# Kernel tuning notes

Hardware: AMD Instinct MI355X
Metric: run time of the kernel (lower is better)

Reference implementation:

```python
import jax, jax.numpy as jnp
import numpy as np

NUM_FIELDS = 40
EMBED_DIM = 128
BATCH = 1024
NUM_IX = NUM_FIELDS * (NUM_FIELDS - 1) // 2  # 780


def _pair_indices(num_fields):
    row, col = [], []
    for i in range(num_fields - 1):
        for j in range(i + 1, num_fields):
            row.append(i)
            col.append(j)
    return np.asarray(row, dtype=np.int32), np.asarray(col, dtype=np.int32)


def setup_inputs() -> dict:
    key = jax.random.key(0)
    k1, k2 = jax.random.split(key)
    x = jax.random.normal(k1, (BATCH, NUM_FIELDS, EMBED_DIM), dtype=jnp.float32)
    # 'mat' kernel: (embed_dim, num_ix, embed_dim), random_normal init
    kernel = jax.random.normal(k2, (EMBED_DIM, NUM_IX, EMBED_DIM), dtype=jnp.float32) * 0.05
    return {"x": x, "kernel": kernel}


def reference(x, kernel) -> jnp.ndarray:
    # x: (B, F, D); kernel: (D, num_ix, D)
    row, col = _pair_indices(x.shape[1])
    p = x[:, row, :]  # (B, num_ix, D)
    q = x[:, col, :]  # (B, num_ix, D)
    # Original: tmp[b,e,n] = sum_d p[b,n,d]*kernel[e,n,d]; kp[b,n] = sum_e tmp[b,e,n]*q[b,n,e]
    # Fused contraction, never materializing the (B, D, num_ix, D) tensor:
    kp = jnp.einsum('bnd,end,bne->bn', p, kernel, q)
    return kp  # (B, num_ix)
```

## Files before the change

### kernel.cpp

```cpp
#include <hip/hip_runtime.h>

#define NF 40
#define ED 128
#define NB 1024
#define NIX 780
#define XROW (NF * ED)
#define KROW (NIX * ED)
#define XB_BYTES (NB * NF * ED * 2)
#define KB_BYTES (NIX * ED * ED * 2)
#define WS_NEED (XB_BYTES + KB_BYTES)

typedef __attribute__((ext_vector_type(8))) short bf16x8;
typedef __attribute__((ext_vector_type(4))) float f32x4;
typedef __attribute__((ext_vector_type(4))) unsigned short ushx4;
typedef __attribute__((ext_vector_type(8))) unsigned short ushx8;

__device__ __forceinline__ unsigned short f2bf(float x) {
  unsigned int u = __float_as_uint(x);
  u = (u + 0x7FFFu + ((u >> 16) & 1u)) >> 16;
  return (unsigned short)u;
}
__device__ __forceinline__ float bf2f(unsigned short h) {
  return __uint_as_float(((unsigned int)h) << 16);
}

#define GLOAD16(gsrc, ldst)                                                    \
  __builtin_amdgcn_global_load_lds(                                            \
      (const __attribute__((address_space(1))) void*)(gsrc),                   \
      (__attribute__((address_space(3))) void*)(ldst), 16, 0, 0)

__global__ void cvt_x(const float* __restrict__ x, unsigned short* __restrict__ xb) {
  const size_t g = ((size_t)blockIdx.x * 256 + threadIdx.x) * 8;
  float4 a = *reinterpret_cast<const float4*>(x + g);
  float4 b = *reinterpret_cast<const float4*>(x + g + 4);
  ushx8 h;
  h[0] = f2bf(a.x); h[1] = f2bf(a.y); h[2] = f2bf(a.z); h[3] = f2bf(a.w);
  h[4] = f2bf(b.x); h[5] = f2bf(b.y); h[6] = f2bf(b.z); h[7] = f2bf(b.w);
  *reinterpret_cast<ushx8*>(xb + g) = h;
}

__global__ void cvt_k(const float* __restrict__ kr, unsigned short* __restrict__ kb) {
  const size_t g = ((size_t)blockIdx.x * 256 + threadIdx.x) * 4;
  const int d = (int)(g & 127);
  const size_t t = g >> 7;
  const int e = (int)(t & 127);
  const int n = (int)(t >> 7);
  float4 v = *reinterpret_cast<const float4*>(kr + ((size_t)e * NIX + n) * ED + d);
  ushx4 h;
  h[0] = f2bf(v.x); h[1] = f2bf(v.y); h[2] = f2bf(v.z); h[3] = f2bf(v.w);
  *reinterpret_cast<ushx4*>(kb + g) = h;
}

__launch_bounds__(256, 2)
__global__ void opn_ws(const unsigned short* __restrict__ xb,
                       const unsigned short* __restrict__ kb,
                       float* __restrict__ out) {
  __shared__ unsigned short S[128 * 128];
  unsigned short* Klds = S;
  unsigned short* Plds = S;
  unsigned short* Qlds = S + 8192;

  const int n = blockIdx.x;
  const int tid = threadIdx.x;
  const int lane = tid & 63;
  const int w = tid >> 6;
  const int lm = lane & 15;
  const int lq = lane >> 4;
  const int col8 = lm * 8;

  int fi = 0, base = 0;
  while (base + (NF - 1 - fi) <= n) { base += NF - 1 - fi; ++fi; }
  const int fj = fi + 1 + (n - base);

  {
    const unsigned short* ks = kb + (size_t)n * (ED * ED);
    #pragma unroll
    for (int j = 0; j < 8; ++j) {
      const int chunk = j * 4 + w;
      const int r = chunk * 4 + lq;
      const int c = col8 ^ ((r & 7) << 3);
      GLOAD16(ks + r * ED + c, Klds + chunk * 512);
    }
  }
  __syncthreads();

  bf16x8 afr[4][8];
  #pragma unroll
  for (int kk = 0; kk < 4; ++kk)
    #pragma unroll
    for (int f = 0; f < 8; ++f) {
      const int r = f * 16 + lm;
      afr[kk][f] = *reinterpret_cast<const bf16x8*>(
          &Klds[r * ED + ((kk * 32 + lq * 8) ^ ((r & 7) << 3))]);
    }
  #pragma unroll
  for (int kk = 0; kk < 4; ++kk)
    #pragma unroll
    for (int f = 0; f < 8; ++f)
      asm volatile("" : "+v"(afr[kk][f]));
  __syncthreads();

  for (int t = 0; t < 8; ++t) {
    const int b0 = blockIdx.y * 512 + t * 64;

    #pragma unroll
    for (int j = 0; j < 4; ++j) {
      const int chunk = j * 4 + w;
      const int r = chunk * 4 + lq;
      const int c = col8 ^ ((r & 7) << 3);
      const size_t xoff = ((size_t)(b0 + r) * NF) * ED + c;
      GLOAD16(xb + xoff + (size_t)fi * ED, Plds + chunk * 512);
      GLOAD16(xb + xoff + (size_t)fj * ED, Qlds + chunk * 512);
    }
    __syncthreads();

    f32x4 acc[8];
    #pragma unroll
    for (int f = 0; f < 8; ++f) acc[f] = (f32x4){0.f, 0.f, 0.f, 0.f};
    const int prow = w * 16 + lm;
    #pragma unroll
    for (int kk = 0; kk < 4; ++kk) {
      bf16x8 pfr = *reinterpret_cast<const bf16x8*>(
          &Plds[prow * ED + ((kk * 32 + lq * 8) ^ ((prow & 7) << 3))]);
      #pragma unroll
      for (int f = 0; f < 8; ++f)
        acc[f] = __builtin_amdgcn_mfma_f32_16x16x32_bf16(afr[kk][f], pfr, acc[f], 0, 0, 0);
    }

    float s = 0.f;
    #pragma unroll
    for (int f = 0; f < 8; ++f) {
      const int c = (f * 16 + lq * 4) ^ ((prow & 7) << 3);
      ushx4 q4 = *reinterpret_cast<const ushx4*>(&Qlds[prow * ED + c]);
      #pragma unroll
      for (int r = 0; r < 4; ++r)
        s = fmaf(acc[f][r], bf2f(q4[r]), s);
    }
    s += __shfl_xor(s, 16);
    s += __shfl_xor(s, 32);
    if (lane < 16) out[(size_t)(b0 + prow) * NIX + n] = s;
    __syncthreads();
  }
}

__device__ __forceinline__ int swz_fb(int row, int col) {
  return row * 128 + (col ^ ((row & 7) << 3));
}

__launch_bounds__(256, 2)
__global__ void opn_fb(const float* __restrict__ x,
                       const float* __restrict__ kern,
                       float* __restrict__ out) {
  __shared__ unsigned short Klds[128 * 128];
  __shared__ unsigned short Plds[64 * 128];
  __shared__ unsigned short Qlds[64 * 132];

  const int n = blockIdx.x;
  const int tid = threadIdx.x;
  const int lane = tid & 63;
  const int w = tid >> 6;
  const int lm = lane & 15;
  const int lq = lane >> 4;

  int fi = 0, base = 0;
  while (base + (NF - 1 - fi) <= n) { base += NF - 1 - fi; ++fi; }
  const int fj = fi + 1 + (n - base);

  {
    const int r8 = tid >> 5;
    const int d0 = (tid & 31) * 4;
    const float* kbp = kern + (size_t)n * ED + d0;
    #pragma unroll
    for (int p = 0; p < 16; ++p) {
      int e = p * 8 + r8;
      float4 v = *reinterpret_cast<const float4*>(kbp + (size_t)e * KROW);
      ushx4 h;
      h[0] = f2bf(v.x); h[1] = f2bf(v.y); h[2] = f2bf(v.z); h[3] = f2bf(v.w);
      *reinterpret_cast<ushx4*>(&Klds[swz_fb(e, d0)]) = h;
    }
  }
  __syncthreads();

  bf16x8 bfr[4][8];
  #pragma unroll
  for (int kk = 0; kk < 4; ++kk)
    #pragma unroll
    for (int f = 0; f < 8; ++f)
      bfr[kk][f] = *reinterpret_cast<const bf16x8*>(
          &Klds[swz_fb(f * 16 + lm, kk * 32 + lq * 8)]);

  const int r8 = tid >> 5;
  const int c4 = (tid & 31) * 4;

  for (int t = 0; t < 8; ++t) {
    const int b0 = blockIdx.y * 512 + t * 64;
    __syncthreads();
    #pragma unroll
    for (int p = 0; p < 8; ++p) {
      int r = p * 8 + r8;
      const float* xbp = x + (size_t)(b0 + r) * XROW + c4;
      float4 vp = *reinterpret_cast<const float4*>(xbp + fi * ED);
      ushx4 hp;
      hp[0] = f2bf(vp.x); hp[1] = f2bf(vp.y); hp[2] = f2bf(vp.z); hp[3] = f2bf(vp.w);
      *reinterpret_cast<ushx4*>(&Plds[swz_fb(r, c4)]) = hp;
      float4 vq = *reinterpret_cast<const float4*>(xbp + fj * ED);
      ushx4 hq;
      hq[0] = f2bf(vq.x); hq[1] = f2bf(vq.y); hq[2] = f2bf(vq.z); hq[3] = f2bf(vq.w);
      *reinterpret_cast<ushx4*>(&Qlds[r * 132 + c4]) = hq;
    }
    __syncthreads();

    f32x4 acc[8];
    #pragma unroll
    for (int f = 0; f < 8; ++f) acc[f] = (f32x4){0.f, 0.f, 0.f, 0.f};
    #pragma unroll
    for (int kk = 0; kk < 4; ++kk) {
      bf16x8 a = *reinterpret_cast<const bf16x8*>(
          &Plds[swz_fb(w * 16 + lm, kk * 32 + lq * 8)]);
      #pragma unroll
      for (int f = 0; f < 8; ++f)
        acc[f] = __builtin_amdgcn_mfma_f32_16x16x32_bf16(a, bfr[kk][f], acc[f], 0, 0, 0);
    }

    #pragma unroll
    for (int r = 0; r < 4; ++r) {
      const int bl = w * 16 + lq * 4 + r;
      float s = 0.f;
      #pragma unroll
      for (int f = 0; f < 8; ++f)
        s = fmaf(acc[f][r], bf2f(Qlds[bl * 132 + f * 16 + lm]), s);
      s += __shfl_xor(s, 1);
      s += __shfl_xor(s, 2);
      s += __shfl_xor(s, 4);
      s += __shfl_xor(s, 8);
      if (lm == 0) out[(size_t)(b0 + bl) * NIX + n] = s;
    }
  }
}

extern "C" void kernel_launch(void* const* d_in, const int* in_sizes, int n_in,
                              void* d_out, int out_size, void* d_ws, size_t ws_size,
                              hipStream_t stream) {
  const float* x = (const float*)d_in[0];
  const float* kern = (const float*)d_in[1];
  float* out = (float*)d_out;
  (void)in_sizes; (void)n_in; (void)out_size;

  if (ws_size >= (size_t)WS_NEED) {
    unsigned short* xb = (unsigned short*)d_ws;
    unsigned short* kbuf = (unsigned short*)((char*)d_ws + XB_BYTES);
    cvt_x<<<2560, 256, 0, stream>>>(x, xb);
    cvt_k<<<12480, 256, 0, stream>>>(kern, kbuf);
    dim3 grid(NIX, 2, 1);
    opn_ws<<<grid, 256, 0, stream>>>(xb, kbuf, out);
  } else {
    dim3 grid(NIX, 2, 1);
    opn_fb<<<grid, 256, 0, stream>>>(x, kern, out);
  }
}
```

Before: 76.26 us.

## Double-buffer P/Q tile loads in LDS to overlap global loads with MFMA

Doubles LDS to two 32KB buffers and software-pipelines the batch-tile loop so the next tile's P/Q rows are loaded asynchronously via global_load_lds while the current tile is computed. It replaces __syncthreads with explicit vmcnt waits and raw barriers, and overlaps the first tile load with the kernel-matrix load. This targets load latency stalls between tiles, at the cost of 64KB LDS per block, which may limit occupancy to the launch-bounds target of 2 blocks and relies on correct vmcnt counting.

```diff
diff --git a/kernel.cpp b/kernel.cpp
--- a/kernel.cpp
+++ b/kernel.cpp
@@ -28,6 +28,15 @@
   __builtin_amdgcn_global_load_lds(                                            \
       (const __attribute__((address_space(1))) void*)(gsrc),                   \
       (__attribute__((address_space(3))) void*)(ldst), 16, 0, 0)
+
+#define WAITV(N) asm volatile("s_waitcnt vmcnt(" #N ")" ::: "memory")
+#define WAITL0() asm volatile("s_waitcnt lgkmcnt(0)" ::: "memory")
+#define BARRIER()                                                              \
+  do {                                                                         \
+    asm volatile("" ::: "memory");                                             \
+    __builtin_amdgcn_s_barrier();                                              \
+    asm volatile("" ::: "memory");                                             \
+  } while (0)
 
 __global__ void cvt_x(const float* __restrict__ x, unsigned short* __restrict__ xb) {
   const size_t g = ((size_t)blockIdx.x * 256 + threadIdx.x) * 8;
@@ -55,10 +64,9 @@
 __global__ void opn_ws(const unsigned short* __restrict__ xb,
                        const unsigned short* __restrict__ kb,
                        float* __restrict__ out) {
-  __shared__ unsigned short S[128 * 128];
-  unsigned short* Klds = S;
-  unsigned short* Plds = S;
-  unsigned short* Qlds = S + 8192;
+  __shared__ unsigned short S[32768];
+  unsigned short* buf0 = S;
+  unsigned short* buf1 = S + 16384;
 
   const int n = blockIdx.x;
   const int tid = threadIdx.x;
@@ -72,6 +80,10 @@
   while (base + (NF - 1 - fi) <= n) { base += NF - 1 - fi; ++fi; }
   const int fj = fi + 1 + (n - base);
 
+  const unsigned short* xpi = xb + (size_t)fi * ED;
+  const unsigned short* xpj = xb + (size_t)fj * ED;
+  const int b0base = blockIdx.y * 512;
+
   {
     const unsigned short* ks = kb + (size_t)n * (ED * ED);
     #pragma unroll
@@ -79,41 +91,48 @@
       const int chunk = j * 4 + w;
       const int r = chunk * 4 + lq;
       const int c = col8 ^ ((r & 7) << 3);
-      GLOAD16(ks + r * ED + c, Klds + chunk * 512);
-    }
-  }
-  __syncthreads();
-
-  bf16x8 afr[4][8];
-  #pragma unroll
-  for (int kk = 0; kk < 4; ++kk)
-    #pragma unroll
-    for (int f = 0; f < 8; ++f) {
-      const int r = f * 16 + lm;
-      afr[kk][f] = *reinterpret_cast<const bf16x8*>(
-          &Klds[r * ED + ((kk * 32 + lq * 8) ^ ((r & 7) << 3))]);
-    }
-  #pragma unroll
-  for (int kk = 0; kk < 4; ++kk)
-    #pragma unroll
-    for (int f = 0; f < 8; ++f)
-      asm volatile("" : "+v"(afr[kk][f]));
-  __syncthreads();
-
-  for (int t = 0; t < 8; ++t) {
-    const int b0 = blockIdx.y * 512 + t * 64;
-
+      GLOAD16(ks + r * ED + c, buf1 + chunk * 512);
+    }
+  }
+
+  auto stage_pq = [&](unsigned short* buf, int t) {
+    const int b0 = b0base + t * 64;
     #pragma unroll
     for (int j = 0; j < 4; ++j) {
       const int chunk = j * 4 + w;
       const int r = chunk * 4 + lq;
       const int c = col8 ^ ((r & 7) << 3);
-      const size_t xoff = ((size_t)(b0 + r) * NF) * ED + c;
-      GLOAD16(xb + xoff + (size_t)fi * ED, Plds + chunk * 512);
-      GLOAD16(xb + xoff + (size_t)fj * ED, Qlds + chunk * 512);
-    }
-    __syncthreads();
-
+      const size_t xoff = (size_t)(b0 + r) * XROW + c;
+      GLOAD16(xpi + xoff, buf + chunk * 512);
+      GLOAD16(xpj + xoff, buf + 8192 + chunk * 512);
+    }
+  };
+
+  stage_pq(buf0, 0);
+  WAITV(8);
+  BARRIER();
+
+  bf16x8 afr[4][8];
+  #pragma unroll
+  for (int kk = 0; kk < 4; ++kk)
+    #pragma unroll
+    for (int f = 0; f < 8; ++f) {
+      const int r = f * 16 + lm;
+      afr[kk][f] = *reinterpret_cast<const bf16x8*>(
+          &buf1[r * ED + ((kk * 32 + lq * 8) ^ ((r & 7) << 3))]);
+    }
+  #pragma unroll
+  for (int kk = 0; kk < 4; ++kk)
+    #pragma unroll
+    for (int f = 0; f < 8; ++f)
+      asm volatile("" : "+v"(afr[kk][f]));
+  WAITL0();
+  BARRIER();
+
+  auto compute = [&](const unsigned short* buf, int t) {
+    const unsigned short* Pl = buf;
+    const unsigned short* Ql = buf + 8192;
+    const int b0 = b0base + t * 64;
     f32x4 acc[8];
     #pragma unroll
     for (int f = 0; f < 8; ++f) acc[f] = (f32x4){0.f, 0.f, 0.f, 0.f};
@@ -121,17 +140,16 @@
     #pragma unroll
     for (int kk = 0; kk < 4; ++kk) {
       bf16x8 pfr = *reinterpret_cast<const bf16x8*>(
-          &Plds[prow * ED + ((kk * 32 + lq * 8) ^ ((prow & 7) << 3))]);
+          &Pl[prow * ED + ((kk * 32 + lq * 8) ^ ((prow & 7) << 3))]);
       #pragma unroll
       for (int f = 0; f < 8; ++f)
         acc[f] = __builtin_amdgcn_mfma_f32_16x16x32_bf16(afr[kk][f], pfr, acc[f], 0, 0, 0);
     }
-
     float s = 0.f;
     #pragma unroll
     for (int f = 0; f < 8; ++f) {
       const int c = (f * 16 + lq * 4) ^ ((prow & 7) << 3);
-      ushx4 q4 = *reinterpret_cast<const ushx4*>(&Qlds[prow * ED + c]);
+      ushx4 q4 = *reinterpret_cast<const ushx4*>(&Ql[prow * ED + c]);
       #pragma unroll
       for (int r = 0; r < 4; ++r)
         s = fmaf(acc[f][r], bf2f(q4[r]), s);
@@ -139,8 +157,29 @@
     s += __shfl_xor(s, 16);
     s += __shfl_xor(s, 32);
     if (lane < 16) out[(size_t)(b0 + prow) * NIX + n] = s;
-    __syncthreads();
-  }
+  };
+
+  #pragma unroll 1
+  for (int t = 0; t < 6; t += 2) {
+    stage_pq(buf1, t + 1);
+    WAITV(8);
+    BARRIER();
+    compute(buf0, t);
+    BARRIER();
+    stage_pq(buf0, t + 2);
+    WAITV(8);
+    BARRIER();
+    compute(buf1, t + 1);
+    BARRIER();
+  }
+  stage_pq(buf1, 7);
+  WAITV(8);
+  BARRIER();
+  compute(buf0, 6);
+  BARRIER();
+  WAITV(0);
+  BARRIER();
+  compute(buf1, 7);
 }
 
 __device__ __forceinline__ int swz_fb(int row, int col) {
```

After: 68.37 us. 10.4% less time.

## Fuse conversion kernels and load P/Q directly from global with register double-buffering

Applied to the files above, without the earlier changes.

Merges the x and kernel bf16 conversion kernels into one launch, removing one kernel launch and the gap between them. In the main kernel, P and Q rows are no longer staged through LDS with barriers. Each lane reads its MFMA operand fragments straight from global memory into registers, and the next batch tile's P fragment is prefetched while the current tile computes. This drops the per-tile __syncthreads and LDS traffic, at the cost of less coalesced global reads and higher register pressure.

```diff
diff --git a/kernel.cpp b/kernel.cpp
--- a/kernel.cpp
+++ b/kernel.cpp
@@ -29,36 +29,35 @@
       (const __attribute__((address_space(1))) void*)(gsrc),                   \
       (__attribute__((address_space(3))) void*)(ldst), 16, 0, 0)
 
-__global__ void cvt_x(const float* __restrict__ x, unsigned short* __restrict__ xb) {
-  const size_t g = ((size_t)blockIdx.x * 256 + threadIdx.x) * 8;
-  float4 a = *reinterpret_cast<const float4*>(x + g);
-  float4 b = *reinterpret_cast<const float4*>(x + g + 4);
-  ushx8 h;
-  h[0] = f2bf(a.x); h[1] = f2bf(a.y); h[2] = f2bf(a.z); h[3] = f2bf(a.w);
-  h[4] = f2bf(b.x); h[5] = f2bf(b.y); h[6] = f2bf(b.z); h[7] = f2bf(b.w);
-  *reinterpret_cast<ushx8*>(xb + g) = h;
-}
-
-__global__ void cvt_k(const float* __restrict__ kr, unsigned short* __restrict__ kb) {
-  const size_t g = ((size_t)blockIdx.x * 256 + threadIdx.x) * 4;
-  const int d = (int)(g & 127);
-  const size_t t = g >> 7;
-  const int e = (int)(t & 127);
-  const int n = (int)(t >> 7);
-  float4 v = *reinterpret_cast<const float4*>(kr + ((size_t)e * NIX + n) * ED + d);
-  ushx4 h;
-  h[0] = f2bf(v.x); h[1] = f2bf(v.y); h[2] = f2bf(v.z); h[3] = f2bf(v.w);
-  *reinterpret_cast<ushx4*>(kb + g) = h;
+__global__ void cvt_fused(const float* __restrict__ x, const float* __restrict__ kr,
+                          unsigned short* __restrict__ xb, unsigned short* __restrict__ kb) {
+  const int blk = blockIdx.x;
+  if (blk < 2560) {
+    const size_t g = ((size_t)blk * 256 + threadIdx.x) * 8;
+    float4 a = *reinterpret_cast<const float4*>(x + g);
+    float4 b = *reinterpret_cast<const float4*>(x + g + 4);
+    ushx8 h;
+    h[0] = f2bf(a.x); h[1] = f2bf(a.y); h[2] = f2bf(a.z); h[3] = f2bf(a.w);
+    h[4] = f2bf(b.x); h[5] = f2bf(b.y); h[6] = f2bf(b.z); h[7] = f2bf(b.w);
+    *reinterpret_cast<ushx8*>(xb + g) = h;
+  } else {
+    const size_t g = ((size_t)(blk - 2560) * 256 + threadIdx.x) * 4;
+    const int d = (int)(g & 127);
+    const size_t t = g >> 7;
+    const int e = (int)(t & 127);
+    const int n = (int)(t >> 7);
+    float4 v = *reinterpret_cast<const float4*>(kr + ((size_t)e * NIX + n) * ED + d);
+    ushx4 h;
+    h[0] = f2bf(v.x); h[1] = f2bf(v.y); h[2] = f2bf(v.z); h[3] = f2bf(v.w);
+    *reinterpret_cast<ushx4*>(kb + g) = h;
+  }
 }
 
 __launch_bounds__(256, 2)
 __global__ void opn_ws(const unsigned short* __restrict__ xb,
                        const unsigned short* __restrict__ kb,
                        float* __restrict__ out) {
-  __shared__ unsigned short S[128 * 128];
-  unsigned short* Klds = S;
-  unsigned short* Plds = S;
-  unsigned short* Qlds = S + 8192;
+  __shared__ unsigned short Klds[ED * ED];
 
   const int n = blockIdx.x;
   const int tid = threadIdx.x;
@@ -66,7 +65,6 @@
   const int w = tid >> 6;
   const int lm = lane & 15;
   const int lq = lane >> 4;
-  const int col8 = lm * 8;
 
   int fi = 0, base = 0;
   while (base + (NF - 1 - fi) <= n) { base += NF - 1 - fi; ++fi; }
@@ -74,6 +72,7 @@
 
   {
     const unsigned short* ks = kb + (size_t)n * (ED * ED);
+    const int col8 = lm * 8;
     #pragma unroll
     for (int j = 0; j < 8; ++j) {
       const int chunk = j * 4 + w;
@@ -98,48 +97,55 @@
     #pragma unroll
     for (int f = 0; f < 8; ++f)
       asm volatile("" : "+v"(afr[kk][f]));
-  __syncthreads();
-
-  for (int t = 0; t < 8; ++t) {
-    const int b0 = blockIdx.y * 512 + t * 64;
-
-    #pragma unroll
-    for (int j = 0; j < 4; ++j) {
-      const int chunk = j * 4 + w;
-      const int r = chunk * 4 + lq;
-      const int c = col8 ^ ((r & 7) << 3);
-      const size_t xoff = ((size_t)(b0 + r) * NF) * ED + c;
-      GLOAD16(xb + xoff + (size_t)fi * ED, Plds + chunk * 512);
-      GLOAD16(xb + xoff + (size_t)fj * ED, Qlds + chunk * 512);
-    }
-    __syncthreads();
+
+  const int prow = w * 16 + lm;
+  const int row0 = blockIdx.y * 512 + prow;
+  const unsigned short* pP = xb + (size_t)fi * ED + (size_t)row0 * XROW + lq * 8;
+  const unsigned short* pQ = xb + (size_t)fj * ED + (size_t)row0 * XROW + lq * 4;
+  float* po = out + (size_t)row0 * NIX + n;
+
+  auto loadP = [&](bf16x8 (&pf)[4], int t) {
+    const unsigned short* p = pP + (size_t)t * (64 * XROW);
+    #pragma unroll
+    for (int kk = 0; kk < 4; ++kk)
+      pf[kk] = *reinterpret_cast<const bf16x8*>(p + kk * 32);
+  };
+
+  auto body = [&](bf16x8 (&pf)[4], int t) {
+    const unsigned short* q = pQ + (size_t)t * (64 * XROW);
+    ushx4 qv[8];
+    #pragma unroll
+    for (int f = 0; f < 8; ++f)
+      qv[f] = *reinterpret_cast<const ushx4*>(q + f * 16);
 
     f32x4 acc[8];
     #pragma unroll
     for (int f = 0; f < 8; ++f) acc[f] = (f32x4){0.f, 0.f, 0.f, 0.f};
-    const int prow = w * 16 + lm;
-    #pragma unroll
-    for (int kk = 0; kk < 4; ++kk) {
-      bf16x8 pfr = *reinterpret_cast<const bf16x8*>(
-          &Plds[prow * ED + ((kk * 32 + lq * 8) ^ ((prow & 7) << 3))]);
+    #pragma unroll
+    for (int kk = 0; kk < 4; ++kk)
       #pragma unroll
       for (int f = 0; f < 8; ++f)
-        acc[f] = __builtin_amdgcn_mfma_f32_16x16x32_bf16(afr[kk][f], pfr, acc[f], 0, 0, 0);
-    }
+        acc[f] = __builtin_amdgcn_mfma_f32_16x16x32_bf16(afr[kk][f], pf[kk], acc[f], 0, 0, 0);
 
     float s = 0.f;
     #pragma unroll
-    for (int f = 0; f < 8; ++f) {
-      const int c = (f * 16 + lq * 4) ^ ((prow & 7) << 3);
-      ushx4 q4 = *reinterpret_cast<const ushx4*>(&Qlds[prow * ED + c]);
+    for (int f = 0; f < 8; ++f)
       #pragma unroll
       for (int r = 0; r < 4; ++r)
-        s = fmaf(acc[f][r], bf2f(q4[r]), s);
-    }
+        s = fmaf(acc[f][r], bf2f(qv[f][r]), s);
     s += __shfl_xor(s, 16);
     s += __shfl_xor(s, 32);
-    if (lane < 16) out[(size_t)(b0 + prow) * NIX + n] = s;
-    __syncthreads();
+    if (lane < 16) po[(size_t)t * (64 * NIX)] = s;
+  };
+
+  bf16x8 pA[4], pB[4];
+  loadP(pA, 0);
+  #pragma unroll 1
+  for (int t = 0; t < 8; t += 2) {
+    loadP(pB, t + 1);
+    body(pA, t);
+    if (t + 2 < 8) loadP(pA, t + 2);
+    body(pB, t + 1);
   }
 }
 
@@ -249,8 +255,7 @@
   if (ws_size >= (size_t)WS_NEED) {
     unsigned short* xb = (unsigned short*)d_ws;
     unsigned short* kbuf = (unsigned short*)((char*)d_ws + XB_BYTES);
-    cvt_x<<<2560, 256, 0, stream>>>(x, xb);
-    cvt_k<<<12480, 256, 0, stream>>>(kern, kbuf);
+    cvt_fused<<<15040, 256, 0, stream>>>(x, kern, xb, kbuf);
     dim3 grid(NIX, 2, 1);
     opn_ws<<<grid, 256, 0, stream>>>(xb, kbuf, out);
   } else {
```

New measurement: 108.4 us. 42.1% more time.

## Split kernel columns across waves, shrink batch tile, fuse conversion launches

Applied to the files above, without the earlier changes.

The two bf16 conversion kernels are merged into one launch that branches on block index, removing one kernel launch and its tail. In the main kernel each wave now keeps only its own 32-row slice of the per-pair kernel matrix in registers instead of all 128 rows. Partial dot products are combined across waves through a small shared scratch array. This cuts register pressure so occupancy can rise to 4 blocks per CU, and the batch tile per block and grid are reshaped so twice as many blocks run. The cost is that each pair's kernel matrix is fetched by twice as many blocks, plus an extra cross-wave reduction with a barrier per tile.

```diff
diff --git a/kernel.cpp b/kernel.cpp
--- a/kernel.cpp
+++ b/kernel.cpp
@@ -29,36 +29,36 @@
       (const __attribute__((address_space(1))) void*)(gsrc),                   \
       (__attribute__((address_space(3))) void*)(ldst), 16, 0, 0)
 
-__global__ void cvt_x(const float* __restrict__ x, unsigned short* __restrict__ xb) {
-  const size_t g = ((size_t)blockIdx.x * 256 + threadIdx.x) * 8;
-  float4 a = *reinterpret_cast<const float4*>(x + g);
-  float4 b = *reinterpret_cast<const float4*>(x + g + 4);
-  ushx8 h;
-  h[0] = f2bf(a.x); h[1] = f2bf(a.y); h[2] = f2bf(a.z); h[3] = f2bf(a.w);
-  h[4] = f2bf(b.x); h[5] = f2bf(b.y); h[6] = f2bf(b.z); h[7] = f2bf(b.w);
-  *reinterpret_cast<ushx8*>(xb + g) = h;
-}
-
-__global__ void cvt_k(const float* __restrict__ kr, unsigned short* __restrict__ kb) {
-  const size_t g = ((size_t)blockIdx.x * 256 + threadIdx.x) * 4;
-  const int d = (int)(g & 127);
-  const size_t t = g >> 7;
-  const int e = (int)(t & 127);
-  const int n = (int)(t >> 7);
-  float4 v = *reinterpret_cast<const float4*>(kr + ((size_t)e * NIX + n) * ED + d);
-  ushx4 h;
-  h[0] = f2bf(v.x); h[1] = f2bf(v.y); h[2] = f2bf(v.z); h[3] = f2bf(v.w);
-  *reinterpret_cast<ushx4*>(kb + g) = h;
-}
-
-__launch_bounds__(256, 2)
+__global__ void cvt_fused(const float* __restrict__ x, const float* __restrict__ kr,
+                          unsigned short* __restrict__ xb, unsigned short* __restrict__ kb) {
+  const int blk = blockIdx.x;
+  if (blk < 2560) {
+    const size_t g = ((size_t)blk * 256 + threadIdx.x) * 8;
+    float4 a = *reinterpret_cast<const float4*>(x + g);
+    float4 b = *reinterpret_cast<const float4*>(x + g + 4);
+    ushx8 h;
+    h[0] = f2bf(a.x); h[1] = f2bf(a.y); h[2] = f2bf(a.z); h[3] = f2bf(a.w);
+    h[4] = f2bf(b.x); h[5] = f2bf(b.y); h[6] = f2bf(b.z); h[7] = f2bf(b.w);
+    *reinterpret_cast<ushx8*>(xb + g) = h;
+  } else {
+    const size_t g = ((size_t)(blk - 2560) * 256 + threadIdx.x) * 4;
+    const int d = (int)(g & 127);
+    const size_t t = g >> 7;
+    const int e = (int)(t & 127);
+    const int n = (int)(t >> 7);
+    float4 v = *reinterpret_cast<const float4*>(kr + ((size_t)e * NIX + n) * ED + d);
+    ushx4 h;
+    h[0] = f2bf(v.x); h[1] = f2bf(v.y); h[2] = f2bf(v.z); h[3] = f2bf(v.w);
+    *reinterpret_cast<ushx4*>(kb + g) = h;
+  }
+}
+
+__launch_bounds__(256, 4)
 __global__ void opn_ws(const unsigned short* __restrict__ xb,
                        const unsigned short* __restrict__ kb,
                        float* __restrict__ out) {
-  __shared__ unsigned short S[128 * 128];
-  unsigned short* Klds = S;
-  unsigned short* Plds = S;
-  unsigned short* Qlds = S + 8192;
+  __shared__ unsigned short S[16384];
+  __shared__ float scratch[4][32];
 
   const int n = blockIdx.x;
   const int tid = threadIdx.x;
@@ -79,67 +79,99 @@
       const int chunk = j * 4 + w;
       const int r = chunk * 4 + lq;
       const int c = col8 ^ ((r & 7) << 3);
-      GLOAD16(ks + r * ED + c, Klds + chunk * 512);
+      GLOAD16(ks + r * ED + c, S + chunk * 512);
     }
   }
   __syncthreads();
 
-  bf16x8 afr[4][8];
+  bf16x8 afr[4][2];
   #pragma unroll
   for (int kk = 0; kk < 4; ++kk)
     #pragma unroll
-    for (int f = 0; f < 8; ++f) {
-      const int r = f * 16 + lm;
+    for (int f = 0; f < 2; ++f) {
+      const int r = w * 32 + f * 16 + lm;
       afr[kk][f] = *reinterpret_cast<const bf16x8*>(
-          &Klds[r * ED + ((kk * 32 + lq * 8) ^ ((r & 7) << 3))]);
+          &S[r * ED + ((kk * 32 + lq * 8) ^ ((r & 7) << 3))]);
     }
   #pragma unroll
   for (int kk = 0; kk < 4; ++kk)
     #pragma unroll
-    for (int f = 0; f < 8; ++f)
+    for (int f = 0; f < 2; ++f)
       asm volatile("" : "+v"(afr[kk][f]));
   __syncthreads();
 
+  unsigned short* Plds = S;
+  unsigned short* Qlds = S + 4096;
+
+  const int b0base = blockIdx.y * 256;
+
+  #pragma unroll 1
   for (int t = 0; t < 8; ++t) {
-    const int b0 = blockIdx.y * 512 + t * 64;
-
-    #pragma unroll
-    for (int j = 0; j < 4; ++j) {
+    const int b0 = b0base + t * 32;
+
+    #pragma unroll
+    for (int j = 0; j < 2; ++j) {
       const int chunk = j * 4 + w;
       const int r = chunk * 4 + lq;
       const int c = col8 ^ ((r & 7) << 3);
-      const size_t xoff = ((size_t)(b0 + r) * NF) * ED + c;
+      const size_t xoff = (size_t)(b0 + r) * XROW + c;
       GLOAD16(xb + xoff + (size_t)fi * ED, Plds + chunk * 512);
       GLOAD16(xb + xoff + (size_t)fj * ED, Qlds + chunk * 512);
     }
     __syncthreads();
 
-    f32x4 acc[8];
-    #pragma unroll
-    for (int f = 0; f < 8; ++f) acc[f] = (f32x4){0.f, 0.f, 0.f, 0.f};
-    const int prow = w * 16 + lm;
+    f32x4 acc[2][2];
+    #pragma unroll
+    for (int f = 0; f < 2; ++f)
+      #pragma unroll
+      for (int nt = 0; nt < 2; ++nt)
+        acc[f][nt] = (f32x4){0.f, 0.f, 0.f, 0.f};
+
+    __builtin_amdgcn_s_setprio(1);
     #pragma unroll
     for (int kk = 0; kk < 4; ++kk) {
-      bf16x8 pfr = *reinterpret_cast<const bf16x8*>(
-          &Plds[prow * ED + ((kk * 32 + lq * 8) ^ ((prow & 7) << 3))]);
-      #pragma unroll
-      for (int f = 0; f < 8; ++f)
-        acc[f] = __builtin_amdgcn_mfma_f32_16x16x32_bf16(afr[kk][f], pfr, acc[f], 0, 0, 0);
-    }
-
-    float s = 0.f;
-    #pragma unroll
-    for (int f = 0; f < 8; ++f) {
-      const int c = (f * 16 + lq * 4) ^ ((prow & 7) << 3);
-      ushx4 q4 = *reinterpret_cast<const ushx4*>(&Qlds[prow * ED + c]);
-      #pragma unroll
-      for (int r = 0; r < 4; ++r)
-        s = fmaf(acc[f][r], bf2f(q4[r]), s);
-    }
-    s += __shfl_xor(s, 16);
-    s += __shfl_xor(s, 32);
-    if (lane < 16) out[(size_t)(b0 + prow) * NIX + n] = s;
-    __syncthreads();
+      #pragma unroll
+      for (int nt = 0; nt < 2; ++nt) {
+        const int pb = nt * 16 + lm;
+        bf16x8 pfr = *reinterpret_cast<const bf16x8*>(
+            &Plds[pb * ED + ((kk * 32 + lq * 8) ^ ((pb & 7) << 3))]);
+        #pragma unroll
+        for (int f = 0; f < 2; ++f)
+          acc[f][nt] = __builtin_amdgcn_mfma_f32_16x16x32_bf16(afr[kk][f], pfr, acc[f][nt], 0, 0, 0);
+      }
+    }
+    __builtin_amdgcn_s_setprio(0);
+
+    float s[2];
+    #pragma unroll
+    for (int nt = 0; nt < 2; ++nt) {
+      const int qrow = nt * 16 + lm;
+      float t0 = 0.f, t1 = 0.f, t2 = 0.f, t3 = 0.f;
+      #pragma unroll
+      for (int f = 0; f < 2; ++f) {
+        const int c = (w * 32 + f * 16 + lq * 4) ^ ((qrow & 7) << 3);
+        ushx4 q4 = *reinterpret_cast<const ushx4*>(&Qlds[qrow * ED + c]);
+        t0 = fmaf(acc[f][nt][0], bf2f(q4[0]), t0);
+        t1 = fmaf(acc[f][nt][1], bf2f(q4[1]), t1);
+        t2 = fmaf(acc[f][nt][2], bf2f(q4[2]), t2);
+        t3 = fmaf(acc[f][nt][3], bf2f(q4[3]), t3);
+      }
+      float sv = (t0 + t1) + (t2 + t3);
+      sv += __shfl_xor(sv, 16);
+      sv += __shfl_xor(sv, 32);
+      s[nt] = sv;
+    }
+    if (lq == 0) {
+      scratch[w][lm] = s[0];
+      scratch[w][16 + lm] = s[1];
+    }
+    __syncthreads();
+
+    if (tid < 32) {
+      const int b = tid;
+      float r = (scratch[0][b] + scratch[1][b]) + (scratch[2][b] + scratch[3][b]);
+      out[(size_t)(b0 + b) * NIX + n] = r;
+    }
   }
 }
 
@@ -249,9 +281,8 @@
   if (ws_size >= (size_t)WS_NEED) {
     unsigned short* xb = (unsigned short*)d_ws;
     unsigned short* kbuf = (unsigned short*)((char*)d_ws + XB_BYTES);
-    cvt_x<<<2560, 256, 0, stream>>>(x, xb);
-    cvt_k<<<12480, 256, 0, stream>>>(kern, kbuf);
-    dim3 grid(NIX, 2, 1);
+    cvt_fused<<<15040, 256, 0, stream>>>(x, kern, xb, kbuf);
+    dim3 grid(NIX, 4, 1);
     opn_ws<<<grid, 256, 0, stream>>>(xb, kbuf, out);
   } else {
     dim3 grid(NIX, 2, 1);
```

New measurement: 74.50 us. 2.3% less time.
